# Performance work log

Hardware: AMD Instinct MI355X
Metric: run time of the kernel (lower is better)

The kernel has to match this reference:

```python
import jax, jax.numpy as jnp
import numpy as np

USER_NUM = 100000
ITEM_NUM = 50000
D = 64
E = 3200000
B = 16384


def setup_inputs() -> dict:
    key = jax.random.key(0)
    ks = jax.random.split(key, 12)
    user = jax.random.randint(ks[0], (B,), 0, USER_NUM)
    item_i = jax.random.randint(ks[1], (B,), 0, ITEM_NUM)
    item_j = jax.random.randint(ks[2], (B,), 0, ITEM_NUM)
    edge_u = jax.random.randint(ks[3], (E,), 0, USER_NUM)
    edge_i = jax.random.randint(ks[4], (E,), 0, ITEM_NUM)
    edge_val = jax.random.uniform(ks[5], (E,), dtype=jnp.float32)
    # nn.init.normal_(std=0.01)
    user_emb = 0.01 * jax.random.normal(ks[6], (USER_NUM, D), dtype=jnp.float32)
    item_emb = 0.01 * jax.random.normal(ks[7], (ITEM_NUM, D), dtype=jnp.float32)
    old_U_emb = 0.01 * jax.random.normal(ks[8], (USER_NUM, D), dtype=jnp.float32)
    old_I_emb = 0.01 * jax.random.normal(ks[9], (ITEM_NUM, D), dtype=jnp.float32)
    n_U = jax.random.uniform(ks[10], (USER_NUM,), dtype=jnp.float32)
    n_U = n_U / jnp.linalg.norm(n_U)  # pre_self normalizes by L2 norm
    n_I = jax.random.uniform(ks[11], (ITEM_NUM,), dtype=jnp.float32)
    n_I = n_I / jnp.linalg.norm(n_I)
    return {"user": user, "item_i": item_i, "item_j": item_j,
            "edge_u": edge_u, "edge_i": edge_i, "edge_val": edge_val,
            "user_emb": user_emb, "item_emb": item_emb,
            "old_U_emb": old_U_emb, "old_I_emb": old_I_emb,
            "n_U": n_U, "n_I": n_I}


def _spmm(seg_ids, gather_ids, vals, x, num_segments):
    # one hop of sparse adjacency @ dense embeddings: gather -> scale -> scatter-add
    msg = vals[:, None] * x[gather_ids]          # [E, D]
    return jax.ops.segment_sum(msg, seg_ids, num_segments=num_segments)


def reference(user, item_i, item_j, edge_u, edge_i, edge_val,
              user_emb, item_emb, old_U_emb, old_I_emb, n_U, n_I):
    # 3-hop LightGCN-style propagation over bipartite graph
    g1u = _spmm(edge_u, edge_i, edge_val, item_emb, USER_NUM)
    g1i = _spmm(edge_i, edge_u, edge_val, user_emb, ITEM_NUM)
    g2u = _spmm(edge_u, edge_i, edge_val, g1i, USER_NUM)
    g2i = _spmm(edge_i, edge_u, edge_val, g1u, ITEM_NUM)
    g3u = _spmm(edge_u, edge_i, edge_val, g2i, USER_NUM)
    g3i = _spmm(edge_i, edge_u, edge_val, g2u, ITEM_NUM)
    gcn_u = user_emb + 0.5 * g1u + (1.0 / 3.0) * g2u + 0.25 * g3u
    gcn_i = item_emb + 0.5 * g1i + (1.0 / 3.0) * g2i + 0.25 * g3i

    # BPR loss
    u = gcn_u[user]
    ii = gcn_i[item_i]
    ij = gcn_i[item_j]
    pred_i = jnp.sum(u * ii, axis=-1)
    pred_j = jnp.sum(u * ij, axis=-1)
    bpr = -jnp.mean(jax.nn.log_sigmoid(pred_i - pred_j))
    reg = 1e-4 * jnp.mean(jnp.sum(u ** 2 + ii ** 2 + ij ** 2, axis=-1))
    loss_bpr = bpr + reg

    # self-distillation loss (loss_self)
    Ud = jnp.linalg.norm(old_U_emb - gcn_u, axis=1)  # [USER_NUM]
    Id = jnp.linalg.norm(old_I_emb - gcn_i, axis=1)  # [ITEM_NUM]
    loss_self = jnp.dot(Ud, n_U) / USER_NUM + jnp.dot(Id, n_I) / ITEM_NUM

    return jnp.stack([loss_bpr, 100.0 * loss_self,
                      jnp.float32(1.0), jnp.float32(1.0)])
```

## Files before the change

### kernel.cpp

```cpp
#include <hip/hip_runtime.h>

#define USER_NUM 100000
#define ITEM_NUM 50000
#define DD 64
#define NEDGE 3200000
#define NB 16384
#define NSLOT 256

#define ATILE 4096
#define NTILE ((NEDGE + ATILE - 1) / ATILE)
#define USH 9
#define ISH 8
#define UBK ((USER_NUM + (1 << USH) - 1) >> USH)
#define IBK ((ITEM_NUM + (1 << ISH) - 1) >> ISH)
#define NBK (UBK + IBK)
#define CPAD 16
#define HIST_GRID 784
#define UHALF (USER_NUM / 2)
#define BCAP 18432
#define IVCAP 1024

#define FP8_SCALE 64.0f

typedef float v2f __attribute__((ext_vector_type(2)));

__device__ __forceinline__ float waveReduceSum(float x) {
#pragma unroll
    for (int off = 32; off > 0; off >>= 1)
        x += __shfl_down(x, off, 64);
    return x;
}

__device__ __forceinline__ unsigned roundbf(unsigned y) {
    return (y + 0x7fffu + ((y >> 16) & 1u)) >> 16;
}

__device__ __forceinline__ void dec8(const uint2 b, float* f) {
    v2f f0 = __builtin_amdgcn_cvt_pk_f32_fp8(b.x, false);
    v2f f1 = __builtin_amdgcn_cvt_pk_f32_fp8(b.x, true);
    v2f f2 = __builtin_amdgcn_cvt_pk_f32_fp8(b.y, false);
    v2f f3 = __builtin_amdgcn_cvt_pk_f32_fp8(b.y, true);
    f[0] = f0.x; f[1] = f0.y; f[2] = f1.x; f[3] = f1.y;
    f[4] = f2.x; f[5] = f2.y; f[6] = f3.x; f[7] = f3.y;
}
__device__ __forceinline__ void fma8p(const uint2 b, const float v, v2f* a) {
    v2f f0 = __builtin_amdgcn_cvt_pk_f32_fp8(b.x, false);
    v2f f1 = __builtin_amdgcn_cvt_pk_f32_fp8(b.x, true);
    v2f f2 = __builtin_amdgcn_cvt_pk_f32_fp8(b.y, false);
    v2f f3 = __builtin_amdgcn_cvt_pk_f32_fp8(b.y, true);
    const v2f vv = {v, v};
    a[0] += vv * f0;
    a[1] += vv * f1;
    a[2] += vv * f2;
    a[3] += vv * f3;
}
__device__ __forceinline__ uint2 pack_fp8x8(const float* a) {
    int lo = 0, hi = 0;
    lo = __builtin_amdgcn_cvt_pk_fp8_f32(a[0], a[1], lo, false);
    lo = __builtin_amdgcn_cvt_pk_fp8_f32(a[2], a[3], lo, true);
    hi = __builtin_amdgcn_cvt_pk_fp8_f32(a[4], a[5], hi, false);
    hi = __builtin_amdgcn_cvt_pk_fp8_f32(a[6], a[7], hi, true);
    return make_uint2((unsigned)lo, (unsigned)hi);
}

__global__ void __launch_bounds__(256) cvt8_kernel(
    const float4* __restrict__ src, uint2* __restrict__ dst, int n8) {
    int t = blockIdx.x * blockDim.x + threadIdx.x;
    if (t < n8) {
        float4 a = src[2 * t], b = src[2 * t + 1];
        float f[8] = {a.x * FP8_SCALE, a.y * FP8_SCALE, a.z * FP8_SCALE, a.w * FP8_SCALE,
                      b.x * FP8_SCALE, b.y * FP8_SCALE, b.z * FP8_SCALE, b.w * FP8_SCALE};
        dst[t] = pack_fp8x8(f);
    }
}


__global__ void __launch_bounds__(256) coarse_hist(
    const int4* __restrict__ eu4, const int4* __restrict__ ei4,
    int* __restrict__ coarseCnt) {
    __shared__ int lc[NBK];
    const int t = threadIdx.x;
    for (int j = t; j < NBK; j += 256) lc[j] = 0;
    __syncthreads();
    for (int k = blockIdx.x * 256 + t; k < NEDGE / 4; k += HIST_GRID * 256) {
        int4 u = eu4[k];
        int4 i = ei4[k];
        atomicAdd(&lc[u.x >> USH], 1); atomicAdd(&lc[u.y >> USH], 1);
        atomicAdd(&lc[u.z >> USH], 1); atomicAdd(&lc[u.w >> USH], 1);
        atomicAdd(&lc[UBK + (i.x >> ISH)], 1); atomicAdd(&lc[UBK + (i.y >> ISH)], 1);
        atomicAdd(&lc[UBK + (i.z >> ISH)], 1); atomicAdd(&lc[UBK + (i.w >> ISH)], 1);
    }
    __syncthreads();
    for (int j = t; j < NBK; j += 256)
        if (lc[j]) atomicAdd(&coarseCnt[j * CPAD], lc[j]);
}

__global__ void __launch_bounds__(512) coarse_scan(
    const int* __restrict__ cnt, int* __restrict__ base, int* __restrict__ cur) {
    __shared__ int a[512];
    const int t = threadIdx.x;
    int v = (t < UBK) ? cnt[t * CPAD] : 0;
    a[t] = v;
    __syncthreads();
    for (int off = 1; off < 512; off <<= 1) {
        int x = (t >= off) ? a[t - off] : 0;
        __syncthreads();
        a[t] += x;
        __syncthreads();
    }
    if (t < UBK) { base[t] = a[t] - v; cur[t * CPAD] = a[t] - v; }
    __syncthreads();
    v = (t < IBK) ? cnt[(UBK + t) * CPAD] : 0;
    a[t] = v;
    __syncthreads();
    for (int off = 1; off < 512; off <<= 1) {
        int x = (t >= off) ? a[t - off] : 0;
        __syncthreads();
        a[t] += x;
        __syncthreads();
    }
    if (t < IBK) { base[UBK + t] = a[t] - v; cur[(UBK + t) * CPAD] = a[t] - v; }
}

__global__ void __launch_bounds__(256, 4) binA(
    const int* __restrict__ eu, const int* __restrict__ ei,
    const float* __restrict__ ev,
    int* __restrict__ ccur,
    int2* __restrict__ stU, int2* __restrict__ stI) {
    __shared__ int2 pay[ATILE];
    __shared__ unsigned char sbid[ATILE];
    __shared__ int hist[256];
    __shared__ int pscan[256];
    __shared__ int cursor[256];
    __shared__ int delta[256];

    const int t = threadIdx.x;
    const int dirI = blockIdx.y;
    const int tb = blockIdx.x * ATILE;
    const int n = min(ATILE, NEDGE - tb);
    const int* key = dirI ? ei : eu;
    const int SH = dirI ? ISH : USH;

    hist[t] = 0;
    __syncthreads();
    for (int k = t; k < n; k += 256)
        atomicAdd(&hist[key[tb + k] >> SH], 1);
    __syncthreads();
    pscan[t] = hist[t];
    __syncthreads();
    for (int off = 1; off < 256; off <<= 1) {
        int x = (t >= off) ? pscan[t - off] : 0;
        __syncthreads();
        pscan[t] += x;
        __syncthreads();
    }
    {
        const int c = hist[t];
        const int lst = pscan[t] - c;
        cursor[t] = lst;
        int gp = 0;
        if (c > 0) {
            int* gc = dirI ? (ccur + UBK * CPAD) : ccur;
            gp = atomicAdd(&gc[t * CPAD], c);
        }
        delta[t] = gp - lst;
    }
    __syncthreads();
    if (dirI == 0) {
        for (int k = t; k < n; k += 256) {
            const int e = tb + k;
            const int u = eu[e], i = ei[e];
            const int b = u >> USH;
            const int p = atomicAdd(&cursor[b], 1);
            pay[p] = make_int2(((u & ((1 << USH) - 1)) << 16) | i,
                               __float_as_int(ev[e]));
            sbid[p] = (unsigned char)b;
        }
    } else {
        for (int k = t; k < n; k += 256) {
            const int e = tb + k;
            const int u = eu[e], i = ei[e];
            const int b = i >> ISH;
            const int p = atomicAdd(&cursor[b], 1);
            pay[p] = make_int2(((i & ((1 << ISH) - 1)) << 17) | u,
                               __float_as_int(ev[e]));
            sbid[p] = (unsigned char)b;
        }
    }
    __syncthreads();
    int2* st = dirI ? stI : stU;
    for (int p = t; p < n; p += 256)
        st[delta[sbid[p]] + p] = pay[p];
}

__global__ void __launch_bounds__(256) binB(
    const int2* __restrict__ stU, const int2* __restrict__ stI,
    const int* __restrict__ base, const int* __restrict__ cnt,
    int* __restrict__ rpU, int* __restrict__ rpI, int* __restrict__ rpIm,
    unsigned* __restrict__ ivU, unsigned* __restrict__ ivI) {
    __shared__ int h[512];
    __shared__ unsigned pay[BCAP];
    const int t = threadIdx.x;
    const int b = blockIdx.x;
    if (b < UBK) {
        const int s = base[b], n = cnt[b * CPAD];
        const int dbase = b << USH;
        h[t] = 0; h[t + 256] = 0;
        __syncthreads();
        for (int p = s + t; p < s + n; p += 256)
            atomicAdd(&h[(unsigned)stU[p].x >> 16], 1);
        __syncthreads();
        const int o0 = h[t], o1 = h[t + 256];
        for (int off = 1; off < 512; off <<= 1) {
            int x0 = (t >= off) ? h[t - off] : 0;
            int x1 = (t + 256 >= off) ? h[t + 256 - off] : 0;
            __syncthreads();
            h[t] += x0; h[t + 256] += x1;
            __syncthreads();
        }
        const int e0 = h[t] - o0, e1 = h[t + 256] - o1;
        __syncthreads();
        h[t] = e0; h[t + 256] = e1;
        if (dbase + t < USER_NUM) rpU[dbase + t] = s + e0;
        if (dbase + 256 + t < USER_NUM) rpU[dbase + 256 + t] = s + e1;
        if (t == 0 && dbase + 512 >= USER_NUM) rpU[USER_NUM] = s + n;
        __syncthreads();
        if (n <= BCAP) {
            for (int p = s + t; p < s + n; p += 256) {
                int2 en = stU[p];
                unsigned x = (unsigned)en.x;
                int pos = atomicAdd(&h[x >> 16], 1);
                unsigned bf = roundbf((unsigned)en.y);
                pay[pos] = (bf << 16) | (x & 0xFFFFu);
            }
            __syncthreads();
            for (int k = t; k < n; k += 256) ivU[s + k] = pay[k];
        } else {
            for (int p = s + t; p < s + n; p += 256) {
                int2 en = stU[p];
                unsigned x = (unsigned)en.x;
                int pos = atomicAdd(&h[x >> 16], 1);
                unsigned bf = roundbf((unsigned)en.y);
                ivU[s + pos] = (bf << 16) | (x & 0xFFFFu);
            }
        }
    } else {
        const int ib = b - UBK;
        const int s = base[b], n = cnt[b * CPAD];
        const int dbase = ib << ISH;
        h[t] = 0; h[t + 256] = 0;
        __syncthreads();
        for (int p = s + t; p < s + n; p += 256) {
            unsigned x = (unsigned)stI[p].x;
            const int c = (int)((x >> 17) << 1) | (((x & 0x1FFFFu) >= UHALF) ? 1 : 0);
            atomicAdd(&h[c], 1);
        }
        __syncthreads();
        const int c0 = h[2 * t], c1 = h[2 * t + 1];
        for (int off = 1; off < 512; off <<= 1) {
            int x0 = (t >= off) ? h[t - off] : 0;
            int x1 = (t + 256 >= off) ? h[t + 256 - off] : 0;
            __syncthreads();
            h[t] += x0; h[t + 256] += x1;
            __syncthreads();
        }
        const int incl0 = h[2 * t], incl1 = h[2 * t + 1];
        const int st0 = incl0 - c0;
        const int st1 = incl1 - c1;
        __syncthreads();
        h[2 * t] = st0; h[2 * t + 1] = st1;
        if (dbase + t < ITEM_NUM) { rpI[dbase + t] = s + st0; rpIm[dbase + t] = s + st1; }
        if (t == 0 && dbase + 256 >= ITEM_NUM) rpI[ITEM_NUM] = s + n;
        __syncthreads();
        if (n <= BCAP) {
            for (int p = s + t; p < s + n; p += 256) {
                int2 en = stI[p];
                unsigned x = (unsigned)en.x;
                const int c = (int)((x >> 17) << 1) | (((x & 0x1FFFFu) >= UHALF) ? 1 : 0);
                int pos = atomicAdd(&h[c], 1);
                unsigned v15 = roundbf((unsigned)en.y) & 0x7FFFu;
                pay[pos] = (v15 << 17) | (x & 0x1FFFFu);
            }
            __syncthreads();
            for (int k = t; k < n; k += 256) ivI[s + k] = pay[k];
        } else {
            for (int p = s + t; p < s + n; p += 256) {
                int2 en = stI[p];
                unsigned x = (unsigned)en.x;
                const int c = (int)((x >> 17) << 1) | (((x & 0x1FFFFu) >= UHALF) ? 1 : 0);
                int pos = atomicAdd(&h[c], 1);
                unsigned v15 = roundbf((unsigned)en.y) & 0x7FFFu;
                ivI[s + pos] = (v15 << 17) | (x & 0x1FFFFu);
            }
        }
    }
}

#define UW (USER_NUM / 8)
#define IW (ITEM_NUM / 8)

template<bool ISU>
__device__ __forceinline__ int xof(unsigned q) {
    return ISU ? (int)(q & 0xFFFFu) : (int)(q & 0x1FFFFu);
}
template<bool ISU>
__device__ __forceinline__ float vof(unsigned q) {
    return ISU ? __uint_as_float(q & 0xFFFF0000u)
               : __uint_as_float((q >> 17) << 16);
}

template<bool ISU, int N>
__device__ __forceinline__ void edge_block(
    const unsigned* __restrict__ iv, int t,
    const uint2* __restrict__ srcr, v2f* a0, v2f* a1) {
    unsigned q[N];
    uint2 b[N];
#pragma unroll
    for (int j = 0; j < N; j++) q[j] = iv[t + j];
#pragma unroll
    for (int j = 0; j < N; j++) b[j] = srcr[xof<ISU>(q[j]) * 8];
#pragma unroll
    for (int j = 0; j < N; j++) fma8p(b[j], vof<ISU>(q[j]), (j & 1) ? a1 : a0);
}

template<bool ISU>
__device__ __forceinline__ void accum_range(
    const unsigned* __restrict__ iv, const uint2* __restrict__ srcr,
    int s, int e2, v2f* a0, v2f* a1) {
    int t = s;
    for (; t + 15 < e2; t += 16) edge_block<ISU, 16>(iv, t, srcr, a0, a1);
    if (t + 7 < e2) { edge_block<ISU, 8>(iv, t, srcr, a0, a1); t += 8; }
    if (t + 3 < e2) { edge_block<ISU, 4>(iv, t, srcr, a0, a1); t += 4; }
    if (t + 1 < e2) { edge_block<ISU, 2>(iv, t, srcr, a0, a1); t += 2; }
    if (t < e2)     edge_block<ISU, 1>(iv, t, srcr, a0, a1);
}

__device__ __forceinline__ void acc_combine(const v2f* a0, const v2f* a1, float* acc) {
#pragma unroll
    for (int k = 0; k < 4; k++) {
        const v2f sv = a0[k] + a1[k];
        acc[2 * k]     = sv.x;
        acc[2 * k + 1] = sv.y;
    }
}

__global__ void __launch_bounds__(256) gather_hop_f8(
    const int* __restrict__ rpU, const unsigned* __restrict__ ivU,
    const uint2* __restrict__ srcForU, uint2* __restrict__ outU,
    const int* __restrict__ rpI, const int* __restrict__ rpIm,
    const unsigned* __restrict__ ivI,
    const uint2* __restrict__ srcForI, uint2* __restrict__ outI) {
    __shared__ unsigned sIv[4][IVCAP];
    const int wslot = threadIdx.x >> 6;
    const int lane = threadIdx.x & 63;
    const int sub = lane >> 3;
    const int r = lane & 7;
    const int wave = blockIdx.x * 4 + wslot;
    const bool active = wave < UW + IW;
    const bool isI = wave < IW;
    int rowBase = 0;
    const int* rp = rpU; const unsigned* ivg = ivU;
    if (active) {
        rowBase = isI ? wave * 8 : (wave - IW) * 8;
        rp  = isI ? rpI : rpU;
        ivg = isI ? ivI : ivU;
    }
    int sB = 0, eB = 0;
    if (active) { sB = rp[rowBase]; eB = rp[rowBase + 8]; }
    unsigned* buf = sIv[wslot];
    const int nst = min(eB - sB, IVCAP);
    for (int k = lane; k < nst; k += 64) buf[k] = ivg[sB + k];
    __syncthreads();
    if (!active) return;
    const int row = rowBase + sub;
    const int sr = rp[row], er = rp[row + 1];
    float acc[8];
    v2f a0[4] = {{0.f,0.f},{0.f,0.f},{0.f,0.f},{0.f,0.f}};
    v2f a1[4] = {{0.f,0.f},{0.f,0.f},{0.f,0.f},{0.f,0.f}};
    if (eB - sB <= IVCAP) {
        const unsigned* p = buf - sB;
        if (isI) {
            const int mr = rpIm[row];
            const uint2* srcr = srcForI + r;
            accum_range<false>(p, srcr, sr, mr, a0, a1);
            accum_range<false>(p, srcr, mr, er, a0, a1);
        } else {
            accum_range<true>(p, srcForU + r, sr, er, a0, a1);
        }
    } else {
        if (isI) {
            const int mr = rpIm[row];
            const uint2* srcr = srcForI + r;
            accum_range<false>(ivg, srcr, sr, mr, a0, a1);
            accum_range<false>(ivg, srcr, mr, er, a0, a1);
        } else {
            accum_range<true>(ivg, srcForU + r, sr, er, a0, a1);
        }
    }
    acc_combine(a0, a1, acc);
    if (isI) outI[row * 8 + r] = pack_fp8x8(acc);
    else     outU[row * 8 + r] = pack_fp8x8(acc);
}

__global__ void __launch_bounds__(256) gather_hop3(
    const int* __restrict__ rpU, const unsigned* __restrict__ ivU,
    const uint2* __restrict__ srcForU,
    const int* __restrict__ rpI, const int* __restrict__ rpIm,
    const unsigned* __restrict__ ivI, const uint2* __restrict__ srcForI,
    const float4* __restrict__ embU, const uint2* __restrict__ g1u,
    const uint2* __restrict__ g2u, float4* __restrict__ gcnU,
    const float4* __restrict__ embI, const uint2* __restrict__ g1i,
    const uint2* __restrict__ g2i, float4* __restrict__ gcnI,
    const float4* __restrict__ oldU4, const float4* __restrict__ oldI4,
    const float* __restrict__ nU, const float* __restrict__ nI,
    float* __restrict__ accs) {
    __shared__ unsigned sIv[4][IVCAP];
    const int wslot = threadIdx.x >> 6;
    const int lane = threadIdx.x & 63;
    const int sub = lane >> 3;
    const int r = lane & 7;
    const int wave = blockIdx.x * 4 + wslot;
    const bool active = wave < UW + IW;
    const bool isI = wave < IW;
    int rowBase = 0;
    const int* rp = rpU; const unsigned* ivg = ivU;
    if (active) {
        rowBase = isI ? wave * 8 : (wave - IW) * 8;
        rp  = isI ? rpI : rpU;
        ivg = isI ? ivI : ivU;
    }
    int sB = 0, eB = 0;
    if (active) { sB = rp[rowBase]; eB = rp[rowBase + 8]; }
    unsigned* buf = sIv[wslot];
    const int nst = min(eB - sB, IVCAP);
    for (int k = lane; k < nst; k += 64) buf[k] = ivg[sB + k];
    __syncthreads();
    if (!active) return;
    const int row = rowBase + sub;
    const int sr = rp[row], er = rp[row + 1];
    float acc[8];
    v2f a0[4] = {{0.f,0.f},{0.f,0.f},{0.f,0.f},{0.f,0.f}};
    v2f a1[4] = {{0.f,0.f},{0.f,0.f},{0.f,0.f},{0.f,0.f}};
    if (eB - sB <= IVCAP) {
        const unsigned* p = buf - sB;
        if (isI) {
            const int mr = rpIm[row];
            const uint2* srcr = srcForI + r;
            accum_range<false>(p, srcr, sr, mr, a0, a1);
            accum_range<false>(p, srcr, mr, er, a0, a1);
        } else {
            accum_range<true>(p, srcForU + r, sr, er, a0, a1);
        }
    } else {
        if (isI) {
            const int mr = rpIm[row];
            const uint2* srcr = srcForI + r;
            accum_range<false>(ivg, srcr, sr, mr, a0, a1);
            accum_range<false>(ivg, srcr, mr, er, a0, a1);
        } else {
            accum_range<true>(ivg, srcForU + r, sr, er, a0, a1);
        }
    }
    acc_combine(a0, a1, acc);
    {
        const float C1 = 0.5f / FP8_SCALE;
        const float C2 = (1.0f / 3.0f) / FP8_SCALE;
        const float C3 = 0.25f / FP8_SCALE;
        const float4* emb  = isI ? embI : embU;
        const uint2*  g1   = isI ? g1i  : g1u;
        const uint2*  g2   = isI ? g2i  : g2u;
        float4*       gcn  = isI ? gcnI : gcnU;
        const float4* old4 = isI ? oldI4 : oldU4;
        const float*  nrm  = isI ? nI   : nU;
        float f1[8], f2[8];
        dec8(g1[row * 8 + r], f1);
        dec8(g2[row * 8 + r], f2);
        const float4 e0 = emb[row * 16 + 2 * r];
        const float4 e1 = emb[row * 16 + 2 * r + 1];
        float4 o0, o1;
        o0.x = e0.x + C1 * f1[0] + C2 * f2[0] + C3 * acc[0];
        o0.y = e0.y + C1 * f1[1] + C2 * f2[1] + C3 * acc[1];
        o0.z = e0.z + C1 * f1[2] + C2 * f2[2] + C3 * acc[2];
        o0.w = e0.w + C1 * f1[3] + C2 * f2[3] + C3 * acc[3];
        o1.x = e1.x + C1 * f1[4] + C2 * f2[4] + C3 * acc[4];
        o1.y = e1.y + C1 * f1[5] + C2 * f2[5] + C3 * acc[5];
        o1.z = e1.z + C1 * f1[6] + C2 * f2[6] + C3 * acc[6];
        o1.w = e1.w + C1 * f1[7] + C2 * f2[7] + C3 * acc[7];
        gcn[row * 16 + 2 * r] = o0;
        gcn[row * 16 + 2 * r + 1] = o1;
        const float4 d0 = old4[row * 16 + 2 * r];
        const float4 d1 = old4[row * 16 + 2 * r + 1];
        const float ex = d0.x - o0.x, ey = d0.y - o0.y;
        const float ez = d0.z - o0.z, ew = d0.w - o0.w;
        const float fx = d1.x - o1.x, fy = d1.y - o1.y;
        const float fz = d1.z - o1.z, fw = d1.w - o1.w;
        float ss = ex * ex + ey * ey + ez * ez + ew * ew
                 + fx * fx + fy * fy + fz * fz + fw * fw;
        ss += __shfl_xor(ss, 1, 64);
        ss += __shfl_xor(ss, 2, 64);
        ss += __shfl_xor(ss, 4, 64);
        float val = (r == 0) ? sqrtf(ss) * nrm[row] : 0.0f;
        val = waveReduceSum(val);
        if (lane == 0) {
            const int slot = wave & (NSLOT - 1);
            unsafeAtomicAdd(&accs[(isI ? 3 : 2) * NSLOT + slot], val);
        }
    }
}

__global__ void __launch_bounds__(256) bpr_loss(
    const int* __restrict__ user, const int* __restrict__ itemI,
    const int* __restrict__ itemJ,
    const float4* __restrict__ gcnU4, const float4* __restrict__ gcnI4,
    float* __restrict__ accs) {
    const int lane = threadIdx.x & 63;
    const int sub = lane >> 4;
    const int r = lane & 15;
    const int W = blockIdx.x * 4 + (threadIdx.x >> 6);
    const int NW = gridDim.x * 4;
    float accB = 0.0f, accR = 0.0f;
    for (int g = W; g < NB / 4; g += NW) {
        const int samp = g * 4 + sub;
        const int uu = user[samp], vi = itemI[samp], vj = itemJ[samp];
        const float4 u  = gcnU4[uu * 16 + r];
        const float4 xi = gcnI4[vi * 16 + r];
        const float4 xj = gcnI4[vj * 16 + r];
        float pi = u.x * xi.x + u.y * xi.y + u.z * xi.z + u.w * xi.w;
        float pj = u.x * xj.x + u.y * xj.y + u.z * xj.z + u.w * xj.w;
        float rg = u.x * u.x + u.y * u.y + u.z * u.z + u.w * u.w
                 + xi.x * xi.x + xi.y * xi.y + xi.z * xi.z + xi.w * xi.w
                 + xj.x * xj.x + xj.y * xj.y + xj.z * xj.z + xj.w * xj.w;
#pragma unroll
        for (int off = 1; off <= 8; off <<= 1) {
            pi += __shfl_xor(pi, off, 64);
            pj += __shfl_xor(pj, off, 64);
            rg += __shfl_xor(rg, off, 64);
        }
        if (r == 0) {
            const float x = pi - pj;
            accB += fmaxf(-x, 0.0f) + log1pf(expf(-fabsf(x)));
            accR += rg;
        }
    }
    accB = waveReduceSum(accB);
    accR = waveReduceSum(accR);
    if (lane == 0) {
        const int slot = W & (NSLOT - 1);
        unsafeAtomicAdd(&accs[0 * NSLOT + slot], accB);
        unsafeAtomicAdd(&accs[1 * NSLOT + slot], accR);
    }
}

__global__ void __launch_bounds__(64) finalize(const float* __restrict__ accs,
                                               float* __restrict__ out) {
    const int lane = threadIdx.x;
    float s[4];
#pragma unroll
    for (int k = 0; k < 4; k++) {
        float v = 0.0f;
        for (int j = lane; j < NSLOT; j += 64) v += accs[k * NSLOT + j];
        s[k] = waveReduceSum(v);
    }
    if (lane == 0) {
        const float loss_bpr = s[0] / NB + 1e-4f * (s[1] / NB);
        const float loss_self = s[2] / USER_NUM + s[3] / ITEM_NUM;
        out[0] = loss_bpr;
        out[1] = 100.0f * loss_self;
        out[2] = 1.0f;
        out[3] = 1.0f;
    }
}

extern "C" void kernel_launch(void* const* d_in, const int* in_sizes, int n_in,
                              void* d_out, int out_size, void* d_ws, size_t ws_size,
                              hipStream_t stream) {
    const int*   user     = (const int*)d_in[0];
    const int*   item_i   = (const int*)d_in[1];
    const int*   item_j   = (const int*)d_in[2];
    const int*   edge_u   = (const int*)d_in[3];
    const int*   edge_i   = (const int*)d_in[4];
    const float* edge_val = (const float*)d_in[5];
    const float* user_emb = (const float*)d_in[6];
    const float* item_emb = (const float*)d_in[7];
    const float* old_U    = (const float*)d_in[8];
    const float* old_I    = (const float*)d_in[9];
    const float* n_U      = (const float*)d_in[10];
    const float* n_I      = (const float*)d_in[11];
    float* out = (float*)d_out;

    char* base = (char*)d_ws;
    size_t off = 0;
    auto carve = [&](size_t bytes) {
        char* p = base + off;
        off += (bytes + 255) & ~(size_t)255;
        return p;
    };
    int*      coarseCnt = (int*)carve(NBK * CPAD * 4);
    float*    accs      = (float*)carve(4 * NSLOT * 4);
    size_t zero_bytes = off;
    int*      cbase = (int*)carve(NBK * 4);
    int*      ccur  = (int*)carve(NBK * CPAD * 4);
    int*      rpU   = (int*)carve((USER_NUM + 1) * 4);
    int*      rpI   = (int*)carve((ITEM_NUM + 1) * 4);
    int*      rpIm  = (int*)carve((ITEM_NUM + 1) * 4);
    unsigned* ivU   = (unsigned*)carve((size_t)NEDGE * 4);
    unsigned* ivI   = (unsigned*)carve((size_t)NEDGE * 4);
    uint2*    ebU8  = (uint2*)carve((size_t)USER_NUM * DD);
    uint2*    ebI8  = (uint2*)carve((size_t)ITEM_NUM * DD);
    uint2*    g1u8  = (uint2*)carve((size_t)USER_NUM * DD);
    uint2*    g1i8  = (uint2*)carve((size_t)ITEM_NUM * DD);
    uint2*    g2u8  = (uint2*)carve((size_t)USER_NUM * DD);
    uint2*    g2i8  = (uint2*)carve((size_t)ITEM_NUM * DD);
    int2*     stU   = (int2*)carve((size_t)NEDGE * 8);
    int2*     stI   = (int2*)carve((size_t)NEDGE * 8);
    float* gcnU = (float*)stU;
    float* gcnI = (float*)stI;

    hipMemsetAsync(d_ws, 0, zero_bytes, stream);

    const dim3 blk(256);

    cvt8_kernel<<<(USER_NUM * 8 + 255) / 256, blk, 0, stream>>>(
        (const float4*)user_emb, ebU8, USER_NUM * 8);
    cvt8_kernel<<<(ITEM_NUM * 8 + 255) / 256, blk, 0, stream>>>(
        (const float4*)item_emb, ebI8, ITEM_NUM * 8);

    coarse_hist<<<HIST_GRID, blk, 0, stream>>>((const int4*)edge_u,
                                               (const int4*)edge_i, coarseCnt);
    coarse_scan<<<1, 512, 0, stream>>>(coarseCnt, cbase, ccur);
    binA<<<dim3(NTILE, 2), blk, 0, stream>>>(edge_u, edge_i, edge_val,
                                             ccur, stU, stI);
    binB<<<NBK, blk, 0, stream>>>(stU, stI, cbase, coarseCnt,
                                  rpU, rpI, rpIm, ivU, ivI);

    const int hop_waves = UW + IW;
    const int hop_grid = (hop_waves + 3) / 4;

    gather_hop_f8<<<hop_grid, blk, 0, stream>>>(rpU, ivU, ebI8, g1u8,
                                                rpI, rpIm, ivI, ebU8, g1i8);
    gather_hop_f8<<<hop_grid, blk, 0, stream>>>(rpU, ivU, g1i8, g2u8,
                                                rpI, rpIm, ivI, g1u8, g2i8);
    gather_hop3<<<hop_grid, blk, 0, stream>>>(
        rpU, ivU, g2i8, rpI, rpIm, ivI, g2u8,
        (const float4*)user_emb, g1u8, g2u8, (float4*)gcnU,
        (const float4*)item_emb, g1i8, g2i8, (float4*)gcnI,
        (const float4*)old_U, (const float4*)old_I, n_U, n_I, accs);

    bpr_loss<<<128, blk, 0, stream>>>(user, item_i, item_j,
                                      (const float4*)gcnU, (const float4*)gcnI, accs);
    finalize<<<1, 64, 0, stream>>>(accs, out);
}
```

Measured before the change: 480.7 us.

## Schedule gather-hop waves in descending edge-count order via counting-sort permutation

```diff
diff --git a/kernel.cpp b/kernel.cpp
--- a/kernel.cpp
+++ b/kernel.cpp
@@ -19,6 +19,12 @@
 #define UHALF (USER_NUM / 2)
 #define BCAP 18432
 #define IVCAP 1024
+
+#define NGRP_U (USER_NUM / 8)
+#define NGRP_I (ITEM_NUM / 8)
+#define NGRP (NGRP_U + NGRP_I)
+#define GBINS 512
+#define GPR 2048
 
 #define FP8_SCALE 64.0f
 
@@ -296,8 +302,76 @@
     }
 }
 
-#define UW (USER_NUM / 8)
-#define IW (ITEM_NUM / 8)
+
+__device__ __forceinline__ int group_weight(
+    int g, const int* __restrict__ rpU, const int* __restrict__ rpI) {
+    if (g < NGRP_U) return rpU[g * 8 + 8] - rpU[g * 8];
+    const int rb = (g - NGRP_U) * 8;
+    return rpI[rb + 8] - rpI[rb];
+}
+__device__ __forceinline__ int group_bin(int w) {
+    return (GBINS - 1) - min(w >> 1, GBINS - 1);
+}
+
+__global__ void __launch_bounds__(256) gperm_hist(
+    const int* __restrict__ rpU, const int* __restrict__ rpI,
+    int* __restrict__ bins) {
+    __shared__ int lb[GBINS];
+    const int t = threadIdx.x;
+    for (int j = t; j < GBINS; j += 256) lb[j] = 0;
+    __syncthreads();
+    for (int g = blockIdx.x * 256 + t; g < NGRP; g += gridDim.x * 256)
+        atomicAdd(&lb[group_bin(group_weight(g, rpU, rpI))], 1);
+    __syncthreads();
+    for (int j = t; j < GBINS; j += 256)
+        if (lb[j]) atomicAdd(&bins[j], lb[j]);
+}
+
+__global__ void __launch_bounds__(512) gperm_scan(
+    const int* __restrict__ bins, int* __restrict__ gcur) {
+    __shared__ int a[GBINS];
+    const int t = threadIdx.x;
+    int v = bins[t];
+    a[t] = v;
+    __syncthreads();
+    for (int off = 1; off < GBINS; off <<= 1) {
+        int x = (t >= off) ? a[t - off] : 0;
+        __syncthreads();
+        a[t] += x;
+        __syncthreads();
+    }
+    gcur[t * CPAD] = a[t] - v;
+}
+
+__global__ void __launch_bounds__(256) gperm_scatter(
+    const int* __restrict__ rpU, const int* __restrict__ rpI,
+    int* __restrict__ gcur, int* __restrict__ gperm) {
+    __shared__ int lh[GBINS], lcur[GBINS], ldelta[GBINS];
+    const int t = threadIdx.x;
+    const int g0 = blockIdx.x * GPR;
+    for (int j = t; j < GBINS; j += 256) { lh[j] = 0; lcur[j] = 0; }
+    __syncthreads();
+    for (int k = t; k < GPR; k += 256) {
+        const int g = g0 + k;
+        if (g < NGRP)
+            atomicAdd(&lh[group_bin(group_weight(g, rpU, rpI))], 1);
+    }
+    __syncthreads();
+    for (int j = t; j < GBINS; j += 256) {
+        const int c = lh[j];
+        ldelta[j] = c ? atomicAdd(&gcur[j * CPAD], c) : 0;
+    }
+    __syncthreads();
+    for (int k = t; k < GPR; k += 256) {
+        const int g = g0 + k;
+        if (g < NGRP) {
+            const int bin = group_bin(group_weight(g, rpU, rpI));
+            const int rank = atomicAdd(&lcur[bin], 1);
+            gperm[ldelta[bin] + rank] = g;
+        }
+    }
+}
+
 
 template<bool ISU>
 __device__ __forceinline__ int xof(unsigned q) {
@@ -349,19 +423,22 @@
     const uint2* __restrict__ srcForU, uint2* __restrict__ outU,
     const int* __restrict__ rpI, const int* __restrict__ rpIm,
     const unsigned* __restrict__ ivI,
-    const uint2* __restrict__ srcForI, uint2* __restrict__ outI) {
+    const uint2* __restrict__ srcForI, uint2* __restrict__ outI,
+    const int* __restrict__ gperm) {
     __shared__ unsigned sIv[4][IVCAP];
     const int wslot = threadIdx.x >> 6;
     const int lane = threadIdx.x & 63;
     const int sub = lane >> 3;
     const int r = lane & 7;
     const int wave = blockIdx.x * 4 + wslot;
-    const bool active = wave < UW + IW;
-    const bool isI = wave < IW;
+    const bool active = wave < NGRP;
+    int grp = 0;
+    if (active) grp = gperm[wave];
+    const bool isI = grp >= NGRP_U;
     int rowBase = 0;
     const int* rp = rpU; const unsigned* ivg = ivU;
     if (active) {
-        rowBase = isI ? wave * 8 : (wave - IW) * 8;
+        rowBase = isI ? (grp - NGRP_U) * 8 : grp * 8;
         rp  = isI ? rpI : rpU;
         ivg = isI ? ivI : ivU;
     }
@@ -413,19 +490,22 @@
     const uint2* __restrict__ g2i, float4* __restrict__ gcnI,
     const float4* __restrict__ oldU4, const float4* __restrict__ oldI4,
     const float* __restrict__ nU, const float* __restrict__ nI,
-    float* __restrict__ accs) {
+    float* __restrict__ accs,
+    const int* __restrict__ gperm) {
     __shared__ unsigned sIv[4][IVCAP];
     const int wslot = threadIdx.x >> 6;
     const int lane = threadIdx.x & 63;
     const int sub = lane >> 3;
     const int r = lane & 7;
     const int wave = blockIdx.x * 4 + wslot;
-    const bool active = wave < UW + IW;
-    const bool isI = wave < IW;
+    const bool active = wave < NGRP;
+    int grp = 0;
+    if (active) grp = gperm[wave];
+    const bool isI = grp >= NGRP_U;
     int rowBase = 0;
     const int* rp = rpU; const unsigned* ivg = ivU;
     if (active) {
-        rowBase = isI ? wave * 8 : (wave - IW) * 8;
+        rowBase = isI ? (grp - NGRP_U) * 8 : grp * 8;
         rp  = isI ? rpI : rpU;
         ivg = isI ? ivI : ivU;
     }
@@ -597,9 +677,12 @@
     };
     int*      coarseCnt = (int*)carve(NBK * CPAD * 4);
     float*    accs      = (float*)carve(4 * NSLOT * 4);
+    int*      gbins     = (int*)carve(GBINS * 4);
     size_t zero_bytes = off;
     int*      cbase = (int*)carve(NBK * 4);
     int*      ccur  = (int*)carve(NBK * CPAD * 4);
+    int*      gcur  = (int*)carve(GBINS * CPAD * 4);
+    int*      gperm = (int*)carve(NGRP * 4);
     int*      rpU   = (int*)carve((USER_NUM + 1) * 4);
     int*      rpI   = (int*)carve((ITEM_NUM + 1) * 4);
     int*      rpIm  = (int*)carve((ITEM_NUM + 1) * 4);
@@ -633,18 +716,25 @@
     binB<<<NBK, blk, 0, stream>>>(stU, stI, cbase, coarseCnt,
                                   rpU, rpI, rpIm, ivU, ivI);
 
-    const int hop_waves = UW + IW;
-    const int hop_grid = (hop_waves + 3) / 4;
+    gperm_hist<<<32, blk, 0, stream>>>(rpU, rpI, gbins);
+    gperm_scan<<<1, 512, 0, stream>>>(gbins, gcur);
+    gperm_scatter<<<(NGRP + GPR - 1) / GPR, blk, 0, stream>>>(rpU, rpI,
+                                                              gcur, gperm);
+
+    const int hop_grid = (NGRP + 3) / 4;
 
     gather_hop_f8<<<hop_grid, blk, 0, stream>>>(rpU, ivU, ebI8, g1u8,
-                                                rpI, rpIm, ivI, ebU8, g1i8);
+                                                rpI, rpIm, ivI, ebU8, g1i8,
+                                                gperm);
     gather_hop_f8<<<hop_grid, blk, 0, stream>>>(rpU, ivU, g1i8, g2u8,
-                                                rpI, rpIm, ivI, g1u8, g2i8);
+                                                rpI, rpIm, ivI, g1u8, g2i8,
+                                                gperm);
     gather_hop3<<<hop_grid, blk, 0, stream>>>(
         rpU, ivU, g2i8, rpI, rpIm, ivI, g2u8,
         (const float4*)user_emb, g1u8, g2u8, (float4*)gcnU,
         (const float4*)item_emb, g1i8, g2i8, (float4*)gcnI,
-        (const float4*)old_U, (const float4*)old_I, n_U, n_I, accs);
+        (const float4*)old_U, (const float4*)old_I, n_U, n_I, accs,
+        gperm);
 
     bpr_loss<<<128, blk, 0, stream>>>(user, item_i, item_j,
                                       (const float4*)gcnU, (const float4*)gcnI, accs);
```

After: 497.5 us. +3.5%, slower.
